# Kernel tuning notes

Hardware: AMD Instinct MI355X
Metric: run time of the kernel (lower is better)

Reference implementation:

```python
import jax, jax.numpy as jnp
import numpy as np

NUM_BUCKETS = 32
MAX_DISTANCE = 128
NUM_HEADS = 16
D_KV = 64


def _relative_position_bucket(relative_position):
    # bidirectional buckets, faithful to T5Attention._relative_position_bucket
    num_buckets = NUM_BUCKETS // 2
    relative_buckets = (relative_position > 0).astype(jnp.int32) * num_buckets
    relative_position = jnp.abs(relative_position)
    max_exact = num_buckets // 2
    is_small = relative_position < max_exact
    rp_f = relative_position.astype(jnp.float32)
    rel_if_large = max_exact + (
        jnp.log(rp_f / max_exact) / np.log(MAX_DISTANCE / max_exact) * (num_buckets - max_exact)
    )
    rel_if_large = jnp.minimum(rel_if_large, num_buckets - 1)
    relative_buckets = relative_buckets + jnp.where(is_small, rp_f, rel_if_large).astype(jnp.int32)
    return relative_buckets


def setup_inputs() -> dict:
    key = jax.random.key(0)
    ks = jax.random.split(key, 6)
    B, S, D = 2, 2048, 1024
    inner = NUM_HEADS * D_KV  # 1024
    q_std = (inner * D_KV) ** (-0.5)
    kv_std = inner ** (-0.5)
    return {
        "hidden_states": jax.random.normal(ks[0], (B, S, D), jnp.float32),
        "attention_mask": jnp.ones((B, S), jnp.int32),
        "Wq": jax.random.normal(ks[1], (D, inner), jnp.float32) * q_std,
        "Wk": jax.random.normal(ks[2], (D, inner), jnp.float32) * kv_std,
        "Wv": jax.random.normal(ks[3], (D, inner), jnp.float32) * kv_std,
        "Wo": jax.random.normal(ks[4], (inner, D), jnp.float32) * kv_std,
        "rel_bias": jax.random.normal(ks[5], (NUM_BUCKETS, NUM_HEADS), jnp.float32),
    }


def reference(hidden_states, attention_mask, Wq, Wk, Wv, Wo, rel_bias):
    B, S, D = hidden_states.shape
    H, Dk = NUM_HEADS, D_KV

    q = (hidden_states @ Wq).reshape(B, S, H, Dk)
    k = (hidden_states @ Wk).reshape(B, S, H, Dk)
    v = (hidden_states @ Wv).reshape(B, S, H, Dk)
    q = q / jnp.sqrt(jnp.asarray(Dk, q.dtype))

    scores = jnp.einsum('bthd,bshd->bhts', q, k)  # [B,H,S,S]

    # relative position bias
    pos = jnp.arange(S, dtype=jnp.int32)
    rel_pos = pos[None, :] - pos[:, None]          # memory - context, [S,S]
    buckets = _relative_position_bucket(rel_pos)   # [S,S]
    bias = rel_bias[buckets]                       # [S,S,H]
    scores = scores + bias.transpose(2, 0, 1)[None].astype(scores.dtype)

    mask = attention_mask[:, None, None, :].astype(scores.dtype)
    scores = scores + (1.0 - mask) * jnp.finfo(scores.dtype).min

    attn = jax.nn.softmax(scores, axis=-1)
    out = jnp.einsum('bhts,bshd->bthd', attn, v).reshape(B, S, H * Dk)
    return out @ Wo
```

## Files before the change

kernel.cpp:

```cpp
#include <hip/hip_runtime.h>
#include <hip/hip_bf16.h>
#include <math.h>

typedef __attribute__((ext_vector_type(8))) short bf16x8;
typedef __attribute__((ext_vector_type(4))) short s16x4;
typedef __attribute__((ext_vector_type(4))) float f32x4;

constexpr int cB = 2, cS = 2048, cH = 16, cD = 64, cIn = 1024, cM = 1024;
constexpr float cLog2e = 1.4426950408889634f;

union BfPack { bf16x8 v; short s[8]; };
union BfPack4 { s16x4 v; short s[4]; };

__device__ __forceinline__ short f2bf(float f) {
    union { float f; unsigned u; } v; v.f = f;
    unsigned r = v.u + 0x7fffu + ((v.u >> 16) & 1u);
    return (short)(r >> 16);
}

__device__ __forceinline__ f32x4 mfma16(bf16x8 a, bf16x8 b, f32x4 c) {
    return __builtin_amdgcn_mfma_f32_16x16x32_bf16(a, b, c, 0, 0, 0);
}

__device__ __forceinline__ void async16(const short* g, short* l) {
    __builtin_amdgcn_global_load_lds(
        (const __attribute__((address_space(1))) unsigned*)(uintptr_t)g,
        (__attribute__((address_space(3))) unsigned*)(uintptr_t)l, 16, 0, 0);
}

__global__ void bias_table_kernel(const float* __restrict__ rel_bias,
                                  const int* __restrict__ mask,
                                  float* __restrict__ bt,
                                  float* __restrict__ maskadd) {
    int idx = blockIdx.x * blockDim.x + threadIdx.x;
    if (idx < 4096) maskadd[idx] = (1.0f - (float)mask[idx]) * -3.0e38f;
    if (idx >= 4095) return;
    int delta = idx - 2047;
    int rb = (delta > 0) ? 16 : 0;
    int ar = delta < 0 ? -delta : delta;
    int bucket;
    if (ar < 8) {
        bucket = rb + ar;
    } else {
        float rl = 8.0f + logf((float)ar * 0.125f) * 2.8853900817779268f;
        rl = fminf(rl, 15.0f);
        bucket = rb + (int)rl;
    }
    #pragma unroll
    for (int h = 0; h < cH; h++)
        bt[h * 4096 + 2048 + delta] = rel_bias[bucket * cH + h] * cLog2e;
}

__global__ __launch_bounds__(256) void conv_hidden_kernel(
    const float* __restrict__ h, short* __restrict__ hbf) {
    int t = blockIdx.x * 256 + threadIdx.x;
    const float4* src = (const float4*)h;
    float4 a = src[2 * t], b = src[2 * t + 1];
    BfPack p;
    p.s[0] = f2bf(a.x); p.s[1] = f2bf(a.y); p.s[2] = f2bf(a.z); p.s[3] = f2bf(a.w);
    p.s[4] = f2bf(b.x); p.s[5] = f2bf(b.y); p.s[6] = f2bf(b.z); p.s[7] = f2bf(b.w);
    ((bf16x8*)hbf)[t] = p.v;
}

__global__ __launch_bounds__(256) void conv_wt_kernel(
    const float* __restrict__ Wq, const float* __restrict__ Wk,
    const float* __restrict__ Wv, const float* __restrict__ Wo,
    short* __restrict__ Wt) {
    const int z = blockIdx.z;
    const float* W = (z == 0) ? Wq : (z == 1) ? Wk : (z == 2) ? Wv : Wo;
    const float scale = (z == 0) ? 0.125f * cLog2e : 1.0f;
    const int n0 = blockIdx.x * 64, k0 = blockIdx.y * 64;
    __shared__ short sW[64][72];
    const int t = threadIdx.x;
    const int r = t >> 2, c4 = (t & 3) * 16;
    {
        const float* src = W + (size_t)(k0 + r) * cM + n0 + c4;
        BfPack p[2];
        #pragma unroll
        for (int q = 0; q < 2; q++) {
            float4 x = ((const float4*)src)[2 * q];
            float4 y = ((const float4*)src)[2 * q + 1];
            p[q].s[0] = f2bf(x.x * scale); p[q].s[1] = f2bf(x.y * scale);
            p[q].s[2] = f2bf(x.z * scale); p[q].s[3] = f2bf(x.w * scale);
            p[q].s[4] = f2bf(y.x * scale); p[q].s[5] = f2bf(y.y * scale);
            p[q].s[6] = f2bf(y.z * scale); p[q].s[7] = f2bf(y.w * scale);
        }
        *(bf16x8*)&sW[r][c4] = p[0].v;
        *(bf16x8*)&sW[r][c4 + 8] = p[1].v;
    }
    __syncthreads();
    const int n = t >> 2, kc = (t & 3) * 16;
    BfPack o0, o1;
    #pragma unroll
    for (int j = 0; j < 8; j++) o0.s[j] = sW[kc + j][n];
    #pragma unroll
    for (int j = 0; j < 8; j++) o1.s[j] = sW[kc + 8 + j][n];
    short* dst = Wt + (size_t)z * cM * cIn + (size_t)(n0 + n) * cIn + k0 + kc;
    *(bf16x8*)dst = o0.v;
    *(bf16x8*)(dst + 8) = o1.v;
}

template <bool SWAP>
__device__ __forceinline__ void gemm_core(
    const short* __restrict__ A, const short* __restrict__ Bt,
    short* smem, int m0, int c0, int tid, f32x4 (&acc)[4][4]) {
    short* sA = smem;
    short* sB = smem + 4096;
    const int w = tid >> 6, l = tid & 63;
    const int m16 = l & 15, g = l >> 4;
    const int srow = l >> 2, scol = (l & 3) * 8;
    const int mq = (w & 1) * 64, nq = (w >> 1) * 64;

    for (int k0 = 0; k0 < cIn; k0 += 32) {
        __syncthreads();
        async16(A + (size_t)(m0 + w * 16 + srow) * cIn + k0 + scol,
                sA + w * 512 + l * 8);
        async16(A + (size_t)(m0 + 64 + w * 16 + srow) * cIn + k0 + scol,
                sA + 2048 + w * 512 + l * 8);
        async16(Bt + (size_t)(c0 + w * 16 + srow) * cIn + k0 + scol,
                sB + w * 512 + l * 8);
        async16(Bt + (size_t)(c0 + 64 + w * 16 + srow) * cIn + k0 + scol,
                sB + 2048 + w * 512 + l * 8);
        __syncthreads();
        bf16x8 af[4], bf[4];
        #pragma unroll
        for (int i = 0; i < 4; i++)
            af[i] = *(const bf16x8*)(sA + (mq + i * 16 + m16) * 32 + g * 8);
        #pragma unroll
        for (int j = 0; j < 4; j++)
            bf[j] = *(const bf16x8*)(sB + (nq + j * 16 + m16) * 32 + g * 8);
        #pragma unroll
        for (int i = 0; i < 4; i++)
            #pragma unroll
            for (int j = 0; j < 4; j++)
                acc[i][j] = SWAP ? mfma16(bf[j], af[i], acc[i][j])
                                 : mfma16(af[i], bf[j], acc[i][j]);
    }
}

__global__ __launch_bounds__(256) void gemm_qkv_kernel(
    const short* __restrict__ hbf, const short* __restrict__ Wt,
    short* __restrict__ Qrm, short* __restrict__ Krm, short* __restrict__ VT) {
    const int z = blockIdx.z;
    const short* Bt = Wt + (size_t)z * cM * cIn;
    const int m0 = blockIdx.y * 128, c0 = blockIdx.x * 128;
    __shared__ short smem[8192];
    const int tid = threadIdx.x, w = tid >> 6, l = tid & 63;
    const int m16 = l & 15, g = l >> 4;
    const int mq = (w & 1) * 64, nq = (w >> 1) * 64;
    f32x4 acc[4][4] = {};

    if (z <= 1) {
        gemm_core<false>(hbf, Bt, smem, m0, c0, tid, acc);
        short* dst = (z == 0) ? Qrm : Krm;
        #pragma unroll
        for (int i = 0; i < 4; i++)
            #pragma unroll
            for (int j = 0; j < 4; j++)
                #pragma unroll
                for (int r = 0; r < 4; r++)
                    dst[(size_t)(m0 + mq + i * 16 + g * 4 + r) * cM +
                        c0 + nq + j * 16 + m16] = f2bf(acc[i][j][r]);
    } else {
        gemm_core<true>(hbf, Bt, smem, m0, c0, tid, acc);
        #pragma unroll
        for (int i = 0; i < 4; i++) {
            const int srow_g = m0 + mq + i * 16 + m16;
            const int bb = srow_g >> 11, ss = srow_g & 2047;
            #pragma unroll
            for (int j = 0; j < 4; j++)
                #pragma unroll
                for (int r = 0; r < 4; r++) {
                    const int wcol = c0 + nq + j * 16 + g * 4 + r;
                    VT[(((size_t)bb * cH + (wcol >> 6)) * cD + (wcol & 63)) * cS
                       + ss] = f2bf(acc[i][j][r]);
                }
        }
    }
}

__global__ __launch_bounds__(256) void attn_kernel(
    const short* __restrict__ Qrm, const short* __restrict__ Krm,
    const short* __restrict__ VT, const float* __restrict__ maskadd,
    const float* __restrict__ bias_t, short* __restrict__ ctx) {
    const int b = blockIdx.z, h = blockIdx.y;
    const int q0 = blockIdx.x * 64;
    const short* VTp = VT + ((size_t)b * cH + h) * cS * cD;
    const float* bh = bias_t + h * 4096 + 2048;
    const float* mp = maskadd + b * cS;

    const int tid = threadIdx.x;
    const int wave = tid >> 6, lane = tid & 63;
    const int m16 = lane & 15, g = lane >> 4;

    __shared__ short Kt[64][72];
    __shared__ short Vt[64][72];

    const int q = q0 + wave * 16 + m16;
    const short* qb = Qrm + (size_t)(b * cS + q) * cM + h * cD;
    bf16x8 qf0 = *(const bf16x8*)(qb + g * 8);
    bf16x8 qf1 = *(const bf16x8*)(qb + 32 + g * 8);

    f32x4 o[4] = {};
    f32x4 lacc = {};
    BfPack ones;
    #pragma unroll
    for (int i = 0; i < 8; i++) ones.s[i] = (short)0x3F80;

    const int srow = tid >> 3;
    const int scol = (tid & 7) << 3;
    const int kb = ((scol >> 4) & 1) * 32 + ((scol >> 3) & 1) * 16 +
                   ((scol >> 5) & 1) * 4;
    const short* kbase = Krm + (size_t)b * cS * cM + h * cD;

    bf16x8 kr0 = *(const bf16x8*)(kbase + (size_t)srow * cM + scol);
    bf16x8 kr1 = *(const bf16x8*)(kbase + (size_t)(srow + 32) * cM + scol);
    bf16x8 vr0 = *(const bf16x8*)(VTp + (size_t)srow * cS + scol);
    bf16x8 vr1 = *(const bf16x8*)(VTp + (size_t)(srow + 32) * cS + scol);

    for (int kt = 0; kt < cS; kt += 64) {
        __syncthreads();
        *(bf16x8*)&Kt[srow][scol] = kr0;
        *(bf16x8*)&Kt[srow + 32][scol] = kr1;
        {
            BfPack v0, v1; v0.v = vr0; v1.v = vr1;
            BfPack4 a, b2, c, d;
            #pragma unroll
            for (int i = 0; i < 4; i++) { a.s[i] = v0.s[i]; b2.s[i] = v0.s[4 + i]; }
            #pragma unroll
            for (int i = 0; i < 4; i++) { c.s[i] = v1.s[i]; d.s[i] = v1.s[4 + i]; }
            *(s16x4*)&Vt[srow][kb]          = a.v;
            *(s16x4*)&Vt[srow][kb + 8]      = b2.v;
            *(s16x4*)&Vt[srow + 32][kb]     = c.v;
            *(s16x4*)&Vt[srow + 32][kb + 8] = d.v;
        }
        __syncthreads();

        const int ktn = (kt + 64 < cS) ? kt + 64 : 0;
        kr0 = *(const bf16x8*)(kbase + (size_t)(ktn + srow) * cM + scol);
        kr1 = *(const bf16x8*)(kbase + (size_t)(ktn + srow + 32) * cM + scol);
        vr0 = *(const bf16x8*)(VTp + (size_t)srow * cS + ktn + scol);
        vr1 = *(const bf16x8*)(VTp + (size_t)(srow + 32) * cS + ktn + scol);

        f32x4 s[4];
        #pragma unroll
        for (int st = 0; st < 4; st++) {
            const int keyb = kt + st * 16 + g * 4;
            f32x4 init;
            #pragma unroll
            for (int c = 0; c < 4; c++)
                init[c] = bh[keyb + c - q] + mp[keyb + c];
            bf16x8 klo = *(const bf16x8*)&Kt[st * 16 + m16][g * 8];
            bf16x8 khi = *(const bf16x8*)&Kt[st * 16 + m16][32 + g * 8];
            s[st] = mfma16(khi, qf1, mfma16(klo, qf0, init));
        }

        BfPack pp[2];
        #pragma unroll
        for (int st = 0; st < 4; st++) {
            #pragma unroll
            for (int r = 0; r < 2; r++) {
                float p0 = __builtin_amdgcn_exp2f(s[st][2 * r]);
                float p1 = __builtin_amdgcn_exp2f(s[st][2 * r + 1]);
                __hip_bfloat162 h2 = __float22bfloat162_rn(float2{p0, p1});
                short2 sp = *(short2*)&h2;
                pp[st & 1].s[(st >> 1) * 4 + 2 * r]     = sp.x;
                pp[st & 1].s[(st >> 1) * 4 + 2 * r + 1] = sp.y;
            }
        }

        lacc = mfma16(ones.v, pp[0].v, lacc);
        lacc = mfma16(ones.v, pp[1].v, lacc);

        #pragma unroll
        for (int nt = 0; nt < 4; nt++) {
            bf16x8 vlo = *(const bf16x8*)&Vt[nt * 16 + m16][g * 8];
            bf16x8 vhi = *(const bf16x8*)&Vt[nt * 16 + m16][32 + g * 8];
            o[nt] = mfma16(vlo, pp[0].v, o[nt]);
            o[nt] = mfma16(vhi, pp[1].v, o[nt]);
        }
    }

    const float inv = 1.0f / lacc[0];
    short* cb = ctx + ((size_t)b * cS + q) * cM + h * cD;
    #pragma unroll
    for (int nt = 0; nt < 4; nt++) {
        BfPack4 pk;
        #pragma unroll
        for (int r = 0; r < 4; r++) pk.s[r] = f2bf(o[nt][r] * inv);
        *(s16x4*)(cb + nt * 16 + g * 4) = pk.v;
    }
}

__global__ __launch_bounds__(256) void gemm_o_kernel(
    const short* __restrict__ ctx, const short* __restrict__ WoT,
    float* __restrict__ out) {
    const int m0 = blockIdx.y * 128, c0 = blockIdx.x * 128;
    __shared__ short smem[8192];
    const int tid = threadIdx.x, w = tid >> 6, l = tid & 63;
    const int m16 = l & 15, g = l >> 4;
    const int mq = (w & 1) * 64, nq = (w >> 1) * 64;
    f32x4 acc[4][4] = {};
    gemm_core<false>(ctx, WoT, smem, m0, c0, tid, acc);
    #pragma unroll
    for (int i = 0; i < 4; i++)
        #pragma unroll
        for (int j = 0; j < 4; j++)
            #pragma unroll
            for (int r = 0; r < 4; r++)
                out[(size_t)(m0 + mq + i * 16 + g * 4 + r) * cM +
                    c0 + nq + j * 16 + m16] = acc[i][j][r];
}

extern "C" void kernel_launch(void* const* d_in, const int* in_sizes, int n_in,
                              void* d_out, int out_size, void* d_ws, size_t ws_size,
                              hipStream_t stream) {
    const float* hidden   = (const float*)d_in[0];
    const int*   mask     = (const int*)d_in[1];
    const float* Wq       = (const float*)d_in[2];
    const float* Wk       = (const float*)d_in[3];
    const float* Wv       = (const float*)d_in[4];
    const float* Wo       = (const float*)d_in[5];
    const float* rel_bias = (const float*)d_in[6];
    float* out = (float*)d_out;

    short* hbf_ctx = (short*)d_ws;
    short* Wt  = hbf_ctx + (size_t)4 * 1024 * 1024;
    short* Qrm = Wt  + (size_t)4 * 1024 * 1024;
    short* Krm = Qrm + (size_t)4 * 1024 * 1024;
    short* VT  = Krm + (size_t)4 * 1024 * 1024;
    float* bias_t  = (float*)(VT + (size_t)4 * 1024 * 1024);
    float* maskf   = bias_t + 16 * 4096;

    bias_table_kernel<<<16, 256, 0, stream>>>(rel_bias, mask, bias_t, maskf);
    conv_hidden_kernel<<<2048, 256, 0, stream>>>(hidden, hbf_ctx);
    conv_wt_kernel<<<dim3(16, 16, 4), 256, 0, stream>>>(Wq, Wk, Wv, Wo, Wt);
    gemm_qkv_kernel<<<dim3(8, 32, 3), 256, 0, stream>>>(hbf_ctx, Wt, Qrm, Krm, VT);
    attn_kernel<<<dim3(32, cH, cB), 256, 0, stream>>>(Qrm, Krm, VT, maskf, bias_t,
                                                      hbf_ctx);
    gemm_o_kernel<<<dim3(8, 32), 256, 0, stream>>>(hbf_ctx, Wt + (size_t)3 * 1024 * 1024,
                                                   out);
}
```

Measured before the change: 213.8 us.

## Double-buffer attention K/V tiles and fold mask into V and row-sum

The attention loop now alternates between two LDS buffers, so only one barrier per 64-key tile is needed and the next tile's global loads overlap compute. Relative-bias values are prefetched as vector loads. The additive mask is replaced by multiplying V by the mask in the QKV GEMM epilogue and using a permuted bf16 mask vector in place of the all-ones operand in the row-sum MFMA. V is stored pre-permuted in global memory, which removes the shuffle on LDS store. This changes masking semantics: masked keys still enter exp but are zeroed in both numerator and denominator, which matches the reference only when not every key is masked. The kernel also gains a launch-bounds occupancy hint of 4.

Measured after the change: 231.4 us. +8.3%, slower.

```diff
diff --git a/kernel.cpp b/kernel.cpp
--- a/kernel.cpp
+++ b/kernel.cpp
@@ -10,7 +10,6 @@
 constexpr float cLog2e = 1.4426950408889634f;
 
 union BfPack { bf16x8 v; short s[8]; };
-union BfPack4 { s16x4 v; short s[4]; };
 
 __device__ __forceinline__ short f2bf(float f) {
     union { float f; unsigned u; } v; v.f = f;
@@ -28,12 +27,28 @@
         (__attribute__((address_space(3))) unsigned*)(uintptr_t)l, 16, 0, 0);
 }
 
+__device__ __forceinline__ f32x4 ld_f32x4_a4(const float* p) {
+    f32x4 r;
+    __builtin_memcpy(&r, p, 16);
+    return r;
+}
+
+__device__ __forceinline__ int kappa64(int off) {
+    return ((off >> 4) & 1) * 32 + ((off >> 2) & 3) * 8 +
+           ((off >> 5) & 1) * 4 + (off & 3);
+}
+
 __global__ void bias_table_kernel(const float* __restrict__ rel_bias,
                                   const int* __restrict__ mask,
                                   float* __restrict__ bt,
-                                  float* __restrict__ maskadd) {
+                                  float* __restrict__ maskmul,
+                                  short* __restrict__ mkp) {
     int idx = blockIdx.x * blockDim.x + threadIdx.x;
-    if (idx < 4096) maskadd[idx] = (1.0f - (float)mask[idx]) * -3.0e38f;
+    if (idx < 4096) {
+        float mv = (float)mask[idx];
+        maskmul[idx] = mv;
+        mkp[(idx & ~63) | kappa64(idx & 63)] = f2bf(mv);
+    }
     if (idx >= 4095) return;
     int delta = idx - 2047;
     int rb = (delta > 0) ? 16 : 0;
@@ -140,6 +155,7 @@
 
 __global__ __launch_bounds__(256) void gemm_qkv_kernel(
     const short* __restrict__ hbf, const short* __restrict__ Wt,
+    const float* __restrict__ maskmul,
     short* __restrict__ Qrm, short* __restrict__ Krm, short* __restrict__ VT) {
     const int z = blockIdx.z;
     const short* Bt = Wt + (size_t)z * cM * cIn;
@@ -167,34 +183,73 @@
         for (int i = 0; i < 4; i++) {
             const int srow_g = m0 + mq + i * 16 + m16;
             const int bb = srow_g >> 11, ss = srow_g & 2047;
+            const float sc = maskmul[bb * cS + ss];
+            const int ssp = (ss & ~63) | kappa64(ss & 63);
             #pragma unroll
             for (int j = 0; j < 4; j++)
                 #pragma unroll
                 for (int r = 0; r < 4; r++) {
                     const int wcol = c0 + nq + j * 16 + g * 4 + r;
                     VT[(((size_t)bb * cH + (wcol >> 6)) * cD + (wcol & 63)) * cS
-                       + ss] = f2bf(acc[i][j][r]);
+                       + ssp] = f2bf(acc[i][j][r] * sc);
                 }
         }
     }
 }
 
-__global__ __launch_bounds__(256) void attn_kernel(
+__device__ __forceinline__ void attn_tile(
+    const short* Kt, const short* Vt, const f32x4 (&bias)[4],
+    const short* mkp_kt, bf16x8 qf0, bf16x8 qf1, int m16, int g,
+    f32x4 (&o)[4], f32x4& lacc) {
+    bf16x8 amk0 = *(const bf16x8*)(mkp_kt + g * 8);
+    bf16x8 amk1 = *(const bf16x8*)(mkp_kt + 32 + g * 8);
+    BfPack pp[2];
+    #pragma unroll
+    for (int st = 0; st < 4; st++) {
+        const short* kr = Kt + (st * 16 + m16) * 72 + g * 8;
+        bf16x8 klo = *(const bf16x8*)kr;
+        bf16x8 khi = *(const bf16x8*)(kr + 32);
+        f32x4 s = mfma16(khi, qf1, mfma16(klo, qf0, bias[st]));
+        #pragma unroll
+        for (int r = 0; r < 2; r++) {
+            float p0 = __builtin_amdgcn_exp2f(s[2 * r]);
+            float p1 = __builtin_amdgcn_exp2f(s[2 * r + 1]);
+            __hip_bfloat162 h2 = __float22bfloat162_rn(float2{p0, p1});
+            short2 sp = *(short2*)&h2;
+            pp[st & 1].s[(st >> 1) * 4 + 2 * r]     = sp.x;
+            pp[st & 1].s[(st >> 1) * 4 + 2 * r + 1] = sp.y;
+        }
+    }
+    #pragma unroll
+    for (int nt = 0; nt < 4; nt++) {
+        const short* vr = Vt + (nt * 16 + m16) * 72 + g * 8;
+        bf16x8 vlo = *(const bf16x8*)vr;
+        bf16x8 vhi = *(const bf16x8*)(vr + 32);
+        o[nt] = mfma16(vlo, pp[0].v, o[nt]);
+        o[nt] = mfma16(vhi, pp[1].v, o[nt]);
+    }
+    lacc = mfma16(amk0, pp[0].v, lacc);
+    lacc = mfma16(amk1, pp[1].v, lacc);
+}
+
+__global__ __launch_bounds__(256, 4) void attn_kernel(
     const short* __restrict__ Qrm, const short* __restrict__ Krm,
-    const short* __restrict__ VT, const float* __restrict__ maskadd,
+    const short* __restrict__ VT, const short* __restrict__ mkp,
     const float* __restrict__ bias_t, short* __restrict__ ctx) {
     const int b = blockIdx.z, h = blockIdx.y;
     const int q0 = blockIdx.x * 64;
     const short* VTp = VT + ((size_t)b * cH + h) * cS * cD;
     const float* bh = bias_t + h * 4096 + 2048;
-    const float* mp = maskadd + b * cS;
-
-    const int tid = threadIdx.x;
-    const int wave = tid >> 6, lane = tid & 63;
+    const short* mkb = mkp + b * cS;
+
+    const int tid = threadIdx.x, wave = tid >> 6, lane = tid & 63;
     const int m16 = lane & 15, g = lane >> 4;
 
-    __shared__ short Kt[64][72];
-    __shared__ short Vt[64][72];
+    __shared__ short smem[4 * 64 * 72];
+    short* KtA = smem;
+    short* VtA = smem + 4608;
+    short* KtB = smem + 9216;
+    short* VtB = smem + 13824;
 
     const int q = q0 + wave * 16 + m16;
     const short* qb = Qrm + (size_t)(b * cS + q) * cM + h * cD;
@@ -203,89 +258,68 @@
 
     f32x4 o[4] = {};
     f32x4 lacc = {};
-    BfPack ones;
-    #pragma unroll
-    for (int i = 0; i < 8; i++) ones.s[i] = (short)0x3F80;
-
-    const int srow = tid >> 3;
-    const int scol = (tid & 7) << 3;
-    const int kb = ((scol >> 4) & 1) * 32 + ((scol >> 3) & 1) * 16 +
-                   ((scol >> 5) & 1) * 4;
-    const short* kbase = Krm + (size_t)b * cS * cM + h * cD;
-
-    bf16x8 kr0 = *(const bf16x8*)(kbase + (size_t)srow * cM + scol);
-    bf16x8 kr1 = *(const bf16x8*)(kbase + (size_t)(srow + 32) * cM + scol);
-    bf16x8 vr0 = *(const bf16x8*)(VTp + (size_t)srow * cS + scol);
-    bf16x8 vr1 = *(const bf16x8*)(VTp + (size_t)(srow + 32) * cS + scol);
-
-    for (int kt = 0; kt < cS; kt += 64) {
+
+    const int srow = tid >> 3, scol = (tid & 7) << 3;
+    const short* kp = Krm + (size_t)b * cS * cM + h * cD + (size_t)srow * cM + scol;
+    const short* vp = VTp + (size_t)srow * cS + scol;
+    const float* bq = bh + g * 4 - q;
+
+    bf16x8 kr0, kr1, vr0, vr1;
+    f32x4 bias0[4], bias1[4];
+
+    kr0 = *(const bf16x8*)(kp);
+    kr1 = *(const bf16x8*)(kp + 32 * cM);
+    vr0 = *(const bf16x8*)(vp);
+    vr1 = *(const bf16x8*)(vp + 32 * cS);
+    #pragma unroll
+    for (int st = 0; st < 4; st++) bias0[st] = ld_f32x4_a4(bq + st * 16);
+    *(bf16x8*)(KtA + srow * 72 + scol) = kr0;
+    *(bf16x8*)(KtA + (srow + 32) * 72 + scol) = kr1;
+    *(bf16x8*)(VtA + srow * 72 + scol) = vr0;
+    *(bf16x8*)(VtA + (srow + 32) * 72 + scol) = vr1;
+    kr0 = *(const bf16x8*)(kp + 64 * cM);
+    kr1 = *(const bf16x8*)(kp + 96 * cM);
+    vr0 = *(const bf16x8*)(vp + 64);
+    vr1 = *(const bf16x8*)(vp + 32 * cS + 64);
+    #pragma unroll
+    for (int st = 0; st < 4; st++) bias1[st] = ld_f32x4_a4(bq + 64 + st * 16);
+    __syncthreads();
+
+    for (int kt = 0; kt < cS; kt += 128) {
+        attn_tile(KtA, VtA, bias0, mkb + kt, qf0, qf1, m16, g, o, lacc);
+        *(bf16x8*)(KtB + srow * 72 + scol) = kr0;
+        *(bf16x8*)(KtB + (srow + 32) * 72 + scol) = kr1;
+        *(bf16x8*)(VtB + srow * 72 + scol) = vr0;
+        *(bf16x8*)(VtB + (srow + 32) * 72 + scol) = vr1;
+        kr0 = *(const bf16x8*)(kp + (size_t)(kt + 128) * cM);
+        kr1 = *(const bf16x8*)(kp + (size_t)(kt + 160) * cM);
+        vr0 = *(const bf16x8*)(vp + kt + 128);
+        vr1 = *(const bf16x8*)(vp + 32 * cS + kt + 128);
+        #pragma unroll
+        for (int st = 0; st < 4; st++)
+            bias0[st] = ld_f32x4_a4(bq + kt + 128 + st * 16);
         __syncthreads();
-        *(bf16x8*)&Kt[srow][scol] = kr0;
-        *(bf16x8*)&Kt[srow + 32][scol] = kr1;
-        {
-            BfPack v0, v1; v0.v = vr0; v1.v = vr1;
-            BfPack4 a, b2, c, d;
-            #pragma unroll
-            for (int i = 0; i < 4; i++) { a.s[i] = v0.s[i]; b2.s[i] = v0.s[4 + i]; }
-            #pragma unroll
-            for (int i = 0; i < 4; i++) { c.s[i] = v1.s[i]; d.s[i] = v1.s[4 + i]; }
-            *(s16x4*)&Vt[srow][kb]          = a.v;
-            *(s16x4*)&Vt[srow][kb + 8]      = b2.v;
-            *(s16x4*)&Vt[srow + 32][kb]     = c.v;
-            *(s16x4*)&Vt[srow + 32][kb + 8] = d.v;
-        }
+
+        attn_tile(KtB, VtB, bias1, mkb + kt + 64, qf0, qf1, m16, g, o, lacc);
+        *(bf16x8*)(KtA + srow * 72 + scol) = kr0;
+        *(bf16x8*)(KtA + (srow + 32) * 72 + scol) = kr1;
+        *(bf16x8*)(VtA + srow * 72 + scol) = vr0;
+        *(bf16x8*)(VtA + (srow + 32) * 72 + scol) = vr1;
+        kr0 = *(const bf16x8*)(kp + (size_t)(kt + 192) * cM);
+        kr1 = *(const bf16x8*)(kp + (size_t)(kt + 224) * cM);
+        vr0 = *(const bf16x8*)(vp + kt + 192);
+        vr1 = *(const bf16x8*)(vp + 32 * cS + kt + 192);
+        #pragma unroll
+        for (int st = 0; st < 4; st++)
+            bias1[st] = ld_f32x4_a4(bq + kt + 192 + st * 16);
         __syncthreads();
-
-        const int ktn = (kt + 64 < cS) ? kt + 64 : 0;
-        kr0 = *(const bf16x8*)(kbase + (size_t)(ktn + srow) * cM + scol);
-        kr1 = *(const bf16x8*)(kbase + (size_t)(ktn + srow + 32) * cM + scol);
-        vr0 = *(const bf16x8*)(VTp + (size_t)srow * cS + ktn + scol);
-        vr1 = *(const bf16x8*)(VTp + (size_t)(srow + 32) * cS + ktn + scol);
-
-        f32x4 s[4];
-        #pragma unroll
-        for (int st = 0; st < 4; st++) {
-            const int keyb = kt + st * 16 + g * 4;
-            f32x4 init;
-            #pragma unroll
-            for (int c = 0; c < 4; c++)
-                init[c] = bh[keyb + c - q] + mp[keyb + c];
-            bf16x8 klo = *(const bf16x8*)&Kt[st * 16 + m16][g * 8];
-            bf16x8 khi = *(const bf16x8*)&Kt[st * 16 + m16][32 + g * 8];
-            s[st] = mfma16(khi, qf1, mfma16(klo, qf0, init));
-        }
-
-        BfPack pp[2];
-        #pragma unroll
-        for (int st = 0; st < 4; st++) {
-            #pragma unroll
-            for (int r = 0; r < 2; r++) {
-                float p0 = __builtin_amdgcn_exp2f(s[st][2 * r]);
-                float p1 = __builtin_amdgcn_exp2f(s[st][2 * r + 1]);
-                __hip_bfloat162 h2 = __float22bfloat162_rn(float2{p0, p1});
-                short2 sp = *(short2*)&h2;
-                pp[st & 1].s[(st >> 1) * 4 + 2 * r]     = sp.x;
-                pp[st & 1].s[(st >> 1) * 4 + 2 * r + 1] = sp.y;
-            }
-        }
-
-        lacc = mfma16(ones.v, pp[0].v, lacc);
-        lacc = mfma16(ones.v, pp[1].v, lacc);
-
-        #pragma unroll
-        for (int nt = 0; nt < 4; nt++) {
-            bf16x8 vlo = *(const bf16x8*)&Vt[nt * 16 + m16][g * 8];
-            bf16x8 vhi = *(const bf16x8*)&Vt[nt * 16 + m16][32 + g * 8];
-            o[nt] = mfma16(vlo, pp[0].v, o[nt]);
-            o[nt] = mfma16(vhi, pp[1].v, o[nt]);
-        }
     }
 
     const float inv = 1.0f / lacc[0];
     short* cb = ctx + ((size_t)b * cS + q) * cM + h * cD;
     #pragma unroll
     for (int nt = 0; nt < 4; nt++) {
-        BfPack4 pk;
+        union { s16x4 v; short s[4]; } pk;
         #pragma unroll
         for (int r = 0; r < 4; r++) pk.s[r] = f2bf(o[nt][r] * inv);
         *(s16x4*)(cb + nt * 16 + g * 4) = pk.v;
@@ -330,13 +364,15 @@
     short* Krm = Qrm + (size_t)4 * 1024 * 1024;
     short* VT  = Krm + (size_t)4 * 1024 * 1024;
     float* bias_t  = (float*)(VT + (size_t)4 * 1024 * 1024);
-    float* maskf   = bias_t + 16 * 4096;
-
-    bias_table_kernel<<<16, 256, 0, stream>>>(rel_bias, mask, bias_t, maskf);
+    float* maskmul = bias_t + 16 * 4096;
+    short* mkp     = (short*)(maskmul + 4096);
+
+    bias_table_kernel<<<16, 256, 0, stream>>>(rel_bias, mask, bias_t, maskmul, mkp);
     conv_hidden_kernel<<<2048, 256, 0, stream>>>(hidden, hbf_ctx);
     conv_wt_kernel<<<dim3(16, 16, 4), 256, 0, stream>>>(Wq, Wk, Wv, Wo, Wt);
-    gemm_qkv_kernel<<<dim3(8, 32, 3), 256, 0, stream>>>(hbf_ctx, Wt, Qrm, Krm, VT);
-    attn_kernel<<<dim3(32, cH, cB), 256, 0, stream>>>(Qrm, Krm, VT, maskf, bias_t,
+    gemm_qkv_kernel<<<dim3(8, 32, 3), 256, 0, stream>>>(hbf_ctx, Wt, maskmul,
+                                                        Qrm, Krm, VT);
+    attn_kernel<<<dim3(32, cH, cB), 256, 0, stream>>>(Qrm, Krm, VT, mkp, bias_t,
                                                       hbf_ctx);
     gemm_o_kernel<<<dim3(8, 32), 256, 0, stream>>>(hbf_ctx, Wt + (size_t)3 * 1024 * 1024,
                                                    out);
```
